# Kernel optimization log

Hardware: AMD Instinct MI355X
Metric: run time of the kernel (lower is better)

Reference implementation:

```python
import jax, jax.numpy as jnp
import numpy as np

B, S, D_IN, D_OUT, H = 4, 2048, 1024, 1024, 16
HD = D_OUT // H  # head_dim = 64


def setup_inputs() -> dict:
    key = jax.random.key(0)
    ks = jax.random.split(key, 7)
    sd_in = 1.0 / np.sqrt(D_IN)
    sd_out = 1.0 / np.sqrt(D_OUT)
    return {
        "x": jax.random.normal(ks[0], (B, S, D_IN), dtype=jnp.float32),
        # weights stored [in, out] so y = x @ W (equivalent to torch Linear)
        "wq": jax.random.uniform(ks[1], (D_IN, D_OUT), jnp.float32, -sd_in, sd_in),
        "wk": jax.random.uniform(ks[2], (D_IN, D_OUT), jnp.float32, -sd_in, sd_in),
        "wv": jax.random.uniform(ks[3], (D_IN, D_OUT), jnp.float32, -sd_in, sd_in),
        "wo": jax.random.uniform(ks[4], (D_OUT, D_OUT), jnp.float32, -sd_out, sd_out),
        "bo": jax.random.uniform(ks[5], (D_OUT,), jnp.float32, -sd_out, sd_out),
    }


def reference(x, wq, wk, wv, wo, bo):
    b, n, _ = x.shape
    # project and split heads: [b, h, n, hd]
    q = (x @ wq).reshape(b, n, H, HD).transpose(0, 2, 1, 3)
    k = (x @ wk).reshape(b, n, H, HD).transpose(0, 2, 1, 3)
    v = (x @ wv).reshape(b, n, H, HD).transpose(0, 2, 1, 3)
    scale = 1.0 / jnp.sqrt(jnp.asarray(HD, dtype=x.dtype))
    scores = jnp.einsum('bhqd,bhkd->bhqk', q, k) * scale  # [b,h,n,n]
    causal = jnp.tril(jnp.ones((n, n), dtype=bool))
    scores = jnp.where(causal, scores, -jnp.inf)
    attn = jax.nn.softmax(scores, axis=-1)
    # dropout p=0.0 -> identity
    ctx = jnp.einsum('bhqk,bhkd->bhqd', attn, v)
    ctx = ctx.transpose(0, 2, 1, 3).reshape(b, n, D_OUT)
    return ctx @ wo + bo
```

## Files before the change

### kernel.cpp

```cpp
#include <hip/hip_runtime.h>

#define DEVINL __device__ __forceinline__

typedef __attribute__((ext_vector_type(8))) short s8v;
typedef __attribute__((ext_vector_type(4))) float f4v;
typedef __attribute__((ext_vector_type(16))) float f16v;
typedef __attribute__((ext_vector_type(8))) __bf16 bf8v;
typedef __attribute__((ext_vector_type(4))) unsigned int u4v;

static constexpr int SEQ = 2048;
static constexpr int DIM = 1024;
static constexpr int NH = 16;

DEVINL unsigned short f2bf(float f) {
  unsigned int u = __builtin_bit_cast(unsigned int, f);
  u += 0x7FFFu + ((u >> 16) & 1u);
  return (unsigned short)(u >> 16);
}

DEVINL void gl_lds16(const void* g, void* l) {
  __builtin_amdgcn_global_load_lds((__attribute__((address_space(1))) void*)g,
                                   (__attribute__((address_space(3))) void*)l,
                                   16, 0, 0);
}

DEVINL f4v mfma16(s8v a, s8v b, f4v c) {
  return __builtin_amdgcn_mfma_f32_16x16x32_bf16(__builtin_bit_cast(bf8v, a),
                                                 __builtin_bit_cast(bf8v, b),
                                                 c, 0, 0, 0);
}

DEVINL f16v mfma32(s8v a, s8v b, f16v c) {
  return __builtin_amdgcn_mfma_f32_32x32x16_bf16(__builtin_bit_cast(bf8v, a),
                                                 __builtin_bit_cast(bf8v, b),
                                                 c, 0, 0, 0);
}

DEVINL unsigned cvtpk(float lo, float hi) {
  unsigned r;
  asm("v_cvt_pk_bf16_f32 %0, %1, %2" : "=v"(r) : "v"(lo), "v"(hi));
  return r;
}

DEVINL void plswap(unsigned& a, unsigned& b) {
#if __has_builtin(__builtin_amdgcn_permlane32_swap)
  typedef int i2v __attribute__((ext_vector_type(2)));
  i2v r = __builtin_amdgcn_permlane32_swap((int)a, (int)b, false, false);
  a = (unsigned)r[0]; b = (unsigned)r[1];
#else
  asm volatile("v_permlane32_swap_b32 %0, %1" : "+v"(a), "+v"(b));
#endif
}

DEVINL s8v mkfrag(unsigned w0, unsigned w1, unsigned w2, unsigned w3) {
  u4v t = {w0, w1, w2, w3};
  return __builtin_bit_cast(s8v, t);
}

__global__ __launch_bounds__(256) void k_cvt(const float* __restrict__ in,
                                             unsigned short* __restrict__ outp) {
  const int i = blockIdx.x * 256 + threadIdx.x;
  const f4v* p = (const f4v*)in + (size_t)i * 2;
  f4v a = p[0], b = p[1];
  s8v o;
  o[0] = (short)f2bf(a[0]); o[1] = (short)f2bf(a[1]);
  o[2] = (short)f2bf(a[2]); o[3] = (short)f2bf(a[3]);
  o[4] = (short)f2bf(b[0]); o[5] = (short)f2bf(b[1]);
  o[6] = (short)f2bf(b[2]); o[7] = (short)f2bf(b[3]);
  ((s8v*)outp)[i] = o;
}

__global__ __launch_bounds__(256) void k_twt(const float* __restrict__ w0, const float* __restrict__ w1,
                                             const float* __restrict__ w2, const float* __restrict__ w3,
                                             unsigned short* __restrict__ o0, unsigned short* __restrict__ o1,
                                             unsigned short* __restrict__ o2, unsigned short* __restrict__ o3) {
  __shared__ float tile[32][33];
  const float* w = blockIdx.z == 0 ? w0 : blockIdx.z == 1 ? w1 : blockIdx.z == 2 ? w2 : w3;
  unsigned short* o = blockIdx.z == 0 ? o0 : blockIdx.z == 1 ? o1 : blockIdx.z == 2 ? o2 : o3;
  const int r0 = blockIdx.y * 32, c0 = blockIdx.x * 32;
  const int tx = threadIdx.x & 31, ty = threadIdx.x >> 5;
#pragma unroll
  for (int i = 0; i < 32; i += 8) tile[ty + i][tx] = w[(r0 + ty + i) * DIM + c0 + tx];
  __syncthreads();
#pragma unroll
  for (int i = 0; i < 32; i += 8) o[(c0 + ty + i) * DIM + r0 + tx] = f2bf(tile[tx][ty + i]);
}

DEVINL void stage128(const unsigned short* __restrict__ A, const unsigned short* __restrict__ Bt,
                     int m0, int n0, int k0, char* Ab, char* Bb, int tid) {
#pragma unroll
  for (int ld = 0; ld < 4; ++ld) {
    const int c = ld * 256 + tid;
    const int row = c >> 3;
    const int csw = ((c & 7) ^ (row & 7)) * 8;
    gl_lds16(A + (size_t)(m0 + row) * 1024 + k0 + csw, Ab + c * 16);
    gl_lds16(Bt + (size_t)(n0 + row) * 1024 + k0 + csw, Bb + c * 16);
  }
}

DEVINL void gemm_compute_tile(char* Ar, char* Br, f4v acc[4][4],
                              int l15, int lg, int wm, int wn) {
#pragma unroll
  for (int kk = 0; kk < 2; ++kk) {
    s8v af[4], bfr[4];
    const int kb2 = (kk * 32 + lg * 8) * 2;
#pragma unroll
    for (int mf = 0; mf < 4; ++mf) {
      const int row = wm * 64 + mf * 16 + l15;
      af[mf] = *(const s8v*)(Ar + row * 128 + (kb2 ^ ((row & 7) << 4)));
    }
#pragma unroll
    for (int nf = 0; nf < 4; ++nf) {
      const int row = wn * 64 + nf * 16 + l15;
      bfr[nf] = *(const s8v*)(Br + row * 128 + (kb2 ^ ((row & 7) << 4)));
    }
#pragma unroll
    for (int mf = 0; mf < 4; ++mf)
#pragma unroll
      for (int nf = 0; nf < 4; ++nf) acc[mf][nf] = mfma16(af[mf], bfr[nf], acc[mf][nf]);
  }
}

DEVINL void gemm_ring(const unsigned short* __restrict__ A, const unsigned short* __restrict__ Bt,
                      int m0, int n0, char* smem, f4v acc[4][4]) {
  const int tid = threadIdx.x;
  const int lane = tid & 63, l15 = lane & 15, lg = lane >> 4;
  const int wm = (tid >> 6) >> 1, wn = (tid >> 6) & 1;
  constexpr int NT = 16;

  stage128(A, Bt, m0, n0, 0, smem, smem + 32768, tid);

  for (int t = 0; t < NT - 1; ++t) {
    const int nb = (t + 1) & 1;
    stage128(A, Bt, m0, n0, (t + 1) * 64, smem + nb * 16384, smem + 32768 + nb * 16384, tid);
    asm volatile("s_waitcnt vmcnt(8)" ::: "memory");
    __builtin_amdgcn_s_barrier();
    __builtin_amdgcn_sched_barrier(0);
    const int cb = t & 1;
    gemm_compute_tile(smem + cb * 16384, smem + 32768 + cb * 16384, acc, l15, lg, wm, wn);
    asm volatile("s_waitcnt lgkmcnt(0)" ::: "memory");
    __builtin_amdgcn_sched_barrier(0);
    __builtin_amdgcn_s_barrier();
  }
  asm volatile("s_waitcnt vmcnt(0)" ::: "memory");
  __builtin_amdgcn_s_barrier();
  __builtin_amdgcn_sched_barrier(0);
  gemm_compute_tile(smem + ((NT - 1) & 1) * 16384, smem + 32768 + ((NT - 1) & 1) * 16384,
                    acc, l15, lg, wm, wn);
}

__global__ __launch_bounds__(256) void k_qkv(const unsigned short* __restrict__ xb,
                                             const unsigned short* __restrict__ wqt,
                                             const unsigned short* __restrict__ wkt,
                                             const unsigned short* __restrict__ wvt,
                                             unsigned short* __restrict__ q,
                                             unsigned short* __restrict__ k,
                                             unsigned short* __restrict__ v) {
  __shared__ __align__(16) char smem[65536];
  const int wgid = (blockIdx.x & 7) * 192 + (blockIdx.x >> 3);
  const int m0 = (wgid / 24) * 128;
  const int rem = wgid % 24;
  const int which = rem >> 3;
  const int n0 = (rem & 7) * 128;
  const unsigned short* Bt = which == 0 ? wqt : which == 1 ? wkt : wvt;
  unsigned short* C = which == 0 ? q : which == 1 ? k : v;
  const float oscale = which == 0 ? 0.125f * 1.44269504f : 1.0f;
  f4v acc[4][4];
  const f4v z = {0.f, 0.f, 0.f, 0.f};
#pragma unroll
  for (int a = 0; a < 4; ++a)
#pragma unroll
    for (int b = 0; b < 4; ++b) acc[a][b] = z;
  gemm_ring(xb, Bt, m0, n0, smem, acc);
  const int lane = threadIdx.x & 63, l15 = lane & 15, lg = lane >> 4;
  const int wm = (threadIdx.x >> 6) >> 1, wn = (threadIdx.x >> 6) & 1;
#pragma unroll
  for (int mf = 0; mf < 4; ++mf)
#pragma unroll
    for (int nf = 0; nf < 4; ++nf)
#pragma unroll
      for (int r = 0; r < 4; ++r) {
        const int row = m0 + wm * 64 + mf * 16 + lg * 4 + r;
        const int col = n0 + wn * 64 + nf * 16 + l15;
        C[(size_t)row * 1024 + col] = f2bf(acc[mf][nf][r] * oscale);
      }
}

__global__ __launch_bounds__(256) void k_oproj(const unsigned short* __restrict__ ctx,
                                               const unsigned short* __restrict__ wot,
                                               const float* __restrict__ bo,
                                               float* __restrict__ outp) {
  __shared__ __align__(16) char smem[65536];
  const int wgid = (blockIdx.x & 7) * 64 + (blockIdx.x >> 3);
  const int m0 = (wgid >> 3) * 128;
  const int n0 = (wgid & 7) * 128;
  f4v acc[4][4];
  const f4v z = {0.f, 0.f, 0.f, 0.f};
#pragma unroll
  for (int a = 0; a < 4; ++a)
#pragma unroll
    for (int b = 0; b < 4; ++b) acc[a][b] = z;
  gemm_ring(ctx, wot, m0, n0, smem, acc);
  const int lane = threadIdx.x & 63, l15 = lane & 15, lg = lane >> 4;
  const int wm = (threadIdx.x >> 6) >> 1, wn = (threadIdx.x >> 6) & 1;
#pragma unroll
  for (int nf = 0; nf < 4; ++nf) {
    const int col = n0 + wn * 64 + nf * 16 + l15;
    const float bias = bo[col];
#pragma unroll
    for (int mf = 0; mf < 4; ++mf)
#pragma unroll
      for (int r = 0; r < 4; ++r) {
        const int row = m0 + wm * 64 + mf * 16 + lg * 4 + r;
        outp[(size_t)row * 1024 + col] = acc[mf][nf][r] + bias;
      }
  }
}

__global__ __launch_bounds__(256) void k_tv(const unsigned short* __restrict__ v,
                                            unsigned short* __restrict__ vt) {
  __shared__ unsigned short tile[64][65];
  const int b = blockIdx.z, h = blockIdx.y, s0 = blockIdx.x * 64;
  const int t = threadIdx.x;
#pragma unroll
  for (int i = 0; i < 16; ++i) {
    const int s = i * 4 + (t >> 6), d = t & 63;
    tile[s][d] = v[(size_t)(b * SEQ + s0 + s) * 1024 + h * 64 + d];
  }
  __syncthreads();
#pragma unroll
  for (int i = 0; i < 16; ++i) {
    const int d = i * 4 + (t >> 6), s = t & 63;
    vt[(size_t)((b * NH + h) * 64 + d) * SEQ + s0 + s] = tile[s][d];
  }
}

DEVINL void stage_kv(const unsigned short* __restrict__ kbase,
                     const unsigned short* __restrict__ vbase,
                     int kv0, char* Ks, char* Vs, int tid) {
#pragma unroll
  for (int i = 0; i < 2; ++i) {
    const int c = i * 256 + tid;
    const int row = c >> 3;
    const int csw = ((c & 7) ^ (row & 7)) * 8;
    gl_lds16(kbase + (size_t)(kv0 + row) * 1024 + csw, Ks + c * 16);
    gl_lds16(vbase + (size_t)row * SEQ + kv0 + csw, Vs + c * 16);
  }
}

__global__ __launch_bounds__(256) void k_attn(const unsigned short* __restrict__ q,
                                              const unsigned short* __restrict__ kg,
                                              const unsigned short* __restrict__ vt,
                                              unsigned short* __restrict__ ctx) {
  __shared__ __align__(16) char smem[32768];
  const int b = blockIdx.z, h = blockIdx.y, pair = blockIdx.x;
  const int tid = threadIdx.x, lane = tid & 63, w = tid >> 6;
  const int l31 = lane & 31, hi = lane >> 5;

  const unsigned short* kbase = kg + (size_t)b * SEQ * 1024 + h * 64;
  const unsigned short* vbase = vt + (size_t)((b * NH + h) * 64) * SEQ;

  f16v z16;
#pragma unroll
  for (int i = 0; i < 16; ++i) z16[i] = 0.f;

  for (int seg = 0; seg < 2; ++seg) {
    const int qi = seg == 0 ? pair : 15 - pair;
    const int qbb = qi * 128;
    const int qg = qbb + w * 32 + l31;
    const unsigned short* qp = q + (size_t)(b * SEQ + qg) * 1024 + h * 64;
    s8v qf[4];
#pragma unroll
    for (int kd = 0; kd < 4; ++kd) qf[kd] = *(const s8v*)(qp + kd * 16 + hi * 8);

    f16v o0 = z16, o1 = z16;
    float m = -3e38f, lsum = 0.f;
    const int nt = qi * 2 + 2;

    __syncthreads();
    stage_kv(kbase, vbase, 0, smem, smem + 16384, tid);

    for (int t = 0; t < nt; ++t) {
      const int kv0 = t * 64;
      char* Ks = smem + (t & 1) * 8192;
      char* Vs = smem + 16384 + (t & 1) * 8192;
      __syncthreads();
      if (t + 1 < nt)
        stage_kv(kbase, vbase, kv0 + 64, smem + ((t + 1) & 1) * 8192,
                 smem + 16384 + ((t + 1) & 1) * 8192, tid);
      if (kv0 > qbb + w * 32 + 31) continue;

      f16v s0 = z16, s1 = z16;
#pragma unroll
      for (int kd = 0; kd < 4; ++kd) {
        const int off = kd * 32 + hi * 16;
        const int r0 = l31, r1 = 32 + l31;
        const s8v kf0 = *(const s8v*)(Ks + r0 * 128 + (off ^ ((r0 & 7) << 4)));
        const s8v kf1 = *(const s8v*)(Ks + r1 * 128 + (off ^ ((r1 & 7) << 4)));
        s0 = mfma32(kf0, qf[kd], s0);
        s1 = mfma32(kf1, qf[kd], s1);
      }

      const bool needmask = (kv0 + 63 > qbb + w * 32);
      const int crel = qg - kv0;
      float tmax = -3e38f;
#pragma unroll
      for (int r = 0; r < 16; ++r) {
        const int kvloc = (r & 3) + 8 * (r >> 2) + 4 * hi;
        float v0 = s0[r], v1 = s1[r];
        if (needmask) {
          if (kvloc > crel) v0 = -3e38f;
          if (kvloc + 32 > crel) v1 = -3e38f;
        }
        s0[r] = v0; s1[r] = v1;
        tmax = fmaxf(tmax, fmaxf(v0, v1));
      }
      tmax = fmaxf(tmax, __shfl_xor(tmax, 32));

      const bool grew = tmax > m + 8.f;
      const float mnew = grew ? tmax : m;
      const float corr = __builtin_amdgcn_exp2f(m - mnew);
      m = mnew;

      float rs = 0.f;
#pragma unroll
      for (int r = 0; r < 16; ++r) {
        const float e0 = __builtin_amdgcn_exp2f(s0[r] - m);
        const float e1 = __builtin_amdgcn_exp2f(s1[r] - m);
        s0[r] = e0; s1[r] = e1;
        rs += e0 + e1;
      }
      rs += __shfl_xor(rs, 32);
      lsum = lsum * corr + rs;
      if (__any(grew)) { o0 *= corr; o1 *= corr; }

      unsigned a0 = cvtpk(s0[0], s0[1]), b0 = cvtpk(s0[4], s0[5]); plswap(a0, b0);
      unsigned a1 = cvtpk(s0[2], s0[3]), b1 = cvtpk(s0[6], s0[7]); plswap(a1, b1);
      const s8v f0 = mkfrag(a0, a1, b0, b1);
      unsigned a2 = cvtpk(s0[8], s0[9]), b2 = cvtpk(s0[12], s0[13]); plswap(a2, b2);
      unsigned a3 = cvtpk(s0[10], s0[11]), b3 = cvtpk(s0[14], s0[15]); plswap(a3, b3);
      const s8v f1 = mkfrag(a2, a3, b2, b3);
      unsigned a4 = cvtpk(s1[0], s1[1]), b4 = cvtpk(s1[4], s1[5]); plswap(a4, b4);
      unsigned a5 = cvtpk(s1[2], s1[3]), b5 = cvtpk(s1[6], s1[7]); plswap(a5, b5);
      const s8v f2 = mkfrag(a4, a5, b4, b5);
      unsigned a6 = cvtpk(s1[8], s1[9]), b6 = cvtpk(s1[12], s1[13]); plswap(a6, b6);
      unsigned a7 = cvtpk(s1[10], s1[11]), b7 = cvtpk(s1[14], s1[15]); plswap(a7, b7);
      const s8v f3 = mkfrag(a6, a7, b6, b7);

#pragma unroll
      for (int ks = 0; ks < 4; ++ks) {
        const s8v pb = ks == 0 ? f0 : ks == 1 ? f1 : ks == 2 ? f2 : f3;
        const int off = ks * 32 + hi * 16;
        const int rd0 = l31, rd1 = 32 + l31;
        const s8v v0 = *(const s8v*)(Vs + rd0 * 128 + (off ^ ((rd0 & 7) << 4)));
        const s8v v1 = *(const s8v*)(Vs + rd1 * 128 + (off ^ ((rd1 & 7) << 4)));
        o0 = mfma32(v0, pb, o0);
        o1 = mfma32(v1, pb, o1);
      }
    }

    const float rl = 1.f / lsum;
    unsigned short* crow_p = ctx + (size_t)(b * SEQ + qg) * 1024 + h * 64;
#pragma unroll
    for (int r = 0; r < 16; ++r) {
      const int d = (r & 3) + 8 * (r >> 2) + 4 * hi;
      crow_p[d] = f2bf(o0[r] * rl);
      crow_p[32 + d] = f2bf(o1[r] * rl);
    }
  }
}

extern "C" void kernel_launch(void* const* d_in, const int* in_sizes, int n_in,
                              void* d_out, int out_size, void* d_ws, size_t ws_size,
                              hipStream_t stream) {
  (void)in_sizes; (void)n_in; (void)out_size; (void)ws_size;
  const float* x = (const float*)d_in[0];
  const float* wq = (const float*)d_in[1];
  const float* wk = (const float*)d_in[2];
  const float* wv = (const float*)d_in[3];
  const float* wo = (const float*)d_in[4];
  const float* bo = (const float*)d_in[5];
  float* outp = (float*)d_out;
  char* ws = (char*)d_ws;
  const size_t MB = 1ull << 20;
  unsigned short* xb  = (unsigned short*)(ws + 0 * MB);
  unsigned short* wqt = (unsigned short*)(ws + 16 * MB);
  unsigned short* wkt = (unsigned short*)(ws + 18 * MB);
  unsigned short* wvt = (unsigned short*)(ws + 20 * MB);
  unsigned short* wot = (unsigned short*)(ws + 22 * MB);
  unsigned short* qb_ = (unsigned short*)(ws + 24 * MB);
  unsigned short* kb_ = (unsigned short*)(ws + 40 * MB);
  unsigned short* vb_ = (unsigned short*)(ws + 56 * MB);
  unsigned short* vtb = (unsigned short*)(ws + 72 * MB);
  unsigned short* ctx = (unsigned short*)(ws + 88 * MB);

  k_cvt<<<4096, 256, 0, stream>>>(x, xb);
  k_twt<<<dim3(32, 32, 4), 256, 0, stream>>>(wq, wk, wv, wo, wqt, wkt, wvt, wot);
  k_qkv<<<1536, 256, 0, stream>>>(xb, wqt, wkt, wvt, qb_, kb_, vb_);
  k_tv<<<dim3(32, 16, 4), 256, 0, stream>>>(vb_, vtb);
  k_attn<<<dim3(8, 16, 4), 256, 0, stream>>>(qb_, kb_, vtb, ctx);
  k_oproj<<<512, 256, 0, stream>>>(ctx, wot, bo, outp);
}
```

Baseline: 256.1 us.

## Use 128x256 tiles with 3-stage LDS ring and 8 waves for projection GEMMs

The QKV and output-projection GEMMs move from 128x128 tiles with 256 threads and double buffering to 128x256 tiles with 512 threads (8 waves, 2x4 layout). A triple-buffered 144KB dynamic LDS ring keeps two K-steps in flight, and s_setprio is raised around the MFMA bursts. The goal is more operand reuse per loaded A tile and better hiding of global-to-LDS latency. The cost is that the large LDS footprint allows only one workgroup per CU, and the grid has fewer, larger blocks, which could leave CUs unevenly loaded at the tail.

```diff
diff --git a/kernel.cpp b/kernel.cpp
--- a/kernel.cpp
+++ b/kernel.cpp
@@ -86,82 +86,94 @@
   for (int i = 0; i < 32; i += 8) o[(c0 + ty + i) * DIM + r0 + tx] = f2bf(tile[tx][ty + i]);
 }
 
-DEVINL void stage128(const unsigned short* __restrict__ A, const unsigned short* __restrict__ Bt,
-                     int m0, int n0, int k0, char* Ab, char* Bb, int tid) {
-#pragma unroll
-  for (int ld = 0; ld < 4; ++ld) {
-    const int c = ld * 256 + tid;
+static constexpr int SLOT = 49152;
+static constexpr int RING_LDS = 147456;
+
+DEVINL void stage_ab(const unsigned short* __restrict__ A, const unsigned short* __restrict__ Bt,
+                     int m0, int n0, int k0, char* slot, int tid) {
+#pragma unroll
+  for (int ld = 0; ld < 2; ++ld) {
+    const int c = ld * 512 + tid;
     const int row = c >> 3;
     const int csw = ((c & 7) ^ (row & 7)) * 8;
-    gl_lds16(A + (size_t)(m0 + row) * 1024 + k0 + csw, Ab + c * 16);
-    gl_lds16(Bt + (size_t)(n0 + row) * 1024 + k0 + csw, Bb + c * 16);
-  }
-}
-
-DEVINL void gemm_compute_tile(char* Ar, char* Br, f4v acc[4][4],
-                              int l15, int lg, int wm, int wn) {
-#pragma unroll
-  for (int kk = 0; kk < 2; ++kk) {
-    s8v af[4], bfr[4];
-    const int kb2 = (kk * 32 + lg * 8) * 2;
-#pragma unroll
-    for (int mf = 0; mf < 4; ++mf) {
-      const int row = wm * 64 + mf * 16 + l15;
-      af[mf] = *(const s8v*)(Ar + row * 128 + (kb2 ^ ((row & 7) << 4)));
-    }
-#pragma unroll
-    for (int nf = 0; nf < 4; ++nf) {
-      const int row = wn * 64 + nf * 16 + l15;
-      bfr[nf] = *(const s8v*)(Br + row * 128 + (kb2 ^ ((row & 7) << 4)));
-    }
-#pragma unroll
-    for (int mf = 0; mf < 4; ++mf)
-#pragma unroll
-      for (int nf = 0; nf < 4; ++nf) acc[mf][nf] = mfma16(af[mf], bfr[nf], acc[mf][nf]);
-  }
-}
-
-DEVINL void gemm_ring(const unsigned short* __restrict__ A, const unsigned short* __restrict__ Bt,
-                      int m0, int n0, char* smem, f4v acc[4][4]) {
+    gl_lds16(A + (size_t)(m0 + row) * 1024 + k0 + csw, slot + c * 16);
+  }
+#pragma unroll
+  for (int ld = 0; ld < 4; ++ld) {
+    const int c = ld * 512 + tid;
+    const int row = c >> 3;
+    const int csw = ((c & 7) ^ (row & 7)) * 8;
+    gl_lds16(Bt + (size_t)(n0 + row) * 1024 + k0 + csw, slot + 16384 + c * 16);
+  }
+}
+
+DEVINL void gemm_ring3(const unsigned short* __restrict__ A, const unsigned short* __restrict__ Bt,
+                       int m0, int n0, char* smem, f4v acc[4][4]) {
   const int tid = threadIdx.x;
   const int lane = tid & 63, l15 = lane & 15, lg = lane >> 4;
-  const int wm = (tid >> 6) >> 1, wn = (tid >> 6) & 1;
+  const int wid = tid >> 6, wm = wid >> 2, wn = wid & 3;
   constexpr int NT = 16;
 
-  stage128(A, Bt, m0, n0, 0, smem, smem + 32768, tid);
-
-  for (int t = 0; t < NT - 1; ++t) {
-    const int nb = (t + 1) & 1;
-    stage128(A, Bt, m0, n0, (t + 1) * 64, smem + nb * 16384, smem + 32768 + nb * 16384, tid);
-    asm volatile("s_waitcnt vmcnt(8)" ::: "memory");
+  stage_ab(A, Bt, m0, n0, 0, smem, tid);
+  stage_ab(A, Bt, m0, n0, 64, smem + SLOT, tid);
+
+  for (int t = 0; t < NT; ++t) {
+    if (t + 2 < NT) {
+      stage_ab(A, Bt, m0, n0, (t + 2) * 64, smem + ((t + 2) % 3) * SLOT, tid);
+      asm volatile("s_waitcnt vmcnt(12)" ::: "memory");
+    } else if (t + 2 == NT) {
+      asm volatile("s_waitcnt vmcnt(6)" ::: "memory");
+    } else {
+      asm volatile("s_waitcnt vmcnt(0)" ::: "memory");
+    }
     __builtin_amdgcn_s_barrier();
     __builtin_amdgcn_sched_barrier(0);
-    const int cb = t & 1;
-    gemm_compute_tile(smem + cb * 16384, smem + 32768 + cb * 16384, acc, l15, lg, wm, wn);
-    asm volatile("s_waitcnt lgkmcnt(0)" ::: "memory");
+
+    char* Ar = smem + (t % 3) * SLOT;
+    char* Br = Ar + 16384;
+#pragma unroll
+    for (int kk = 0; kk < 2; ++kk) {
+      s8v af[4];
+#pragma unroll
+      for (int mf = 0; mf < 4; ++mf) {
+        const int row = wm * 64 + mf * 16 + l15;
+        af[mf] = *(const s8v*)(Ar + row * 128 + ((kk * 64 + lg * 16) ^ ((row & 7) << 4)));
+      }
+#pragma unroll
+      for (int nh = 0; nh < 2; ++nh) {
+        s8v bfr[2];
+#pragma unroll
+        for (int j = 0; j < 2; ++j) {
+          const int row = wn * 64 + (nh * 2 + j) * 16 + l15;
+          bfr[j] = *(const s8v*)(Br + row * 128 + ((kk * 64 + lg * 16) ^ ((row & 7) << 4)));
+        }
+        __builtin_amdgcn_s_setprio(1);
+#pragma unroll
+        for (int mf = 0; mf < 4; ++mf) {
+          acc[mf][nh * 2 + 0] = mfma16(af[mf], bfr[0], acc[mf][nh * 2 + 0]);
+          acc[mf][nh * 2 + 1] = mfma16(af[mf], bfr[1], acc[mf][nh * 2 + 1]);
+        }
+        __builtin_amdgcn_s_setprio(0);
+      }
+    }
     __builtin_amdgcn_sched_barrier(0);
     __builtin_amdgcn_s_barrier();
   }
-  asm volatile("s_waitcnt vmcnt(0)" ::: "memory");
-  __builtin_amdgcn_s_barrier();
-  __builtin_amdgcn_sched_barrier(0);
-  gemm_compute_tile(smem + ((NT - 1) & 1) * 16384, smem + 32768 + ((NT - 1) & 1) * 16384,
-                    acc, l15, lg, wm, wn);
-}
-
-__global__ __launch_bounds__(256) void k_qkv(const unsigned short* __restrict__ xb,
-                                             const unsigned short* __restrict__ wqt,
-                                             const unsigned short* __restrict__ wkt,
-                                             const unsigned short* __restrict__ wvt,
-                                             unsigned short* __restrict__ q,
-                                             unsigned short* __restrict__ k,
-                                             unsigned short* __restrict__ v) {
-  __shared__ __align__(16) char smem[65536];
-  const int wgid = (blockIdx.x & 7) * 192 + (blockIdx.x >> 3);
-  const int m0 = (wgid / 24) * 128;
-  const int rem = wgid % 24;
-  const int which = rem >> 3;
-  const int n0 = (rem & 7) * 128;
+}
+
+__global__ __launch_bounds__(512, 2) void k_qkv(const unsigned short* __restrict__ xb,
+                                                const unsigned short* __restrict__ wqt,
+                                                const unsigned short* __restrict__ wkt,
+                                                const unsigned short* __restrict__ wvt,
+                                                unsigned short* __restrict__ q,
+                                                unsigned short* __restrict__ k,
+                                                unsigned short* __restrict__ v) {
+  extern __shared__ __align__(16) char smem[];
+  const int wgid = (blockIdx.x & 7) * 96 + (blockIdx.x >> 3);
+  const int m0 = (wgid / 12) * 128;
+  const int rem = wgid % 12;
+  const int which = rem >> 2;
+  const int n0 = (rem & 3) * 256;
   const unsigned short* Bt = which == 0 ? wqt : which == 1 ? wkt : wvt;
   unsigned short* C = which == 0 ? q : which == 1 ? k : v;
   const float oscale = which == 0 ? 0.125f * 1.44269504f : 1.0f;
@@ -171,9 +183,9 @@
   for (int a = 0; a < 4; ++a)
 #pragma unroll
     for (int b = 0; b < 4; ++b) acc[a][b] = z;
-  gemm_ring(xb, Bt, m0, n0, smem, acc);
+  gemm_ring3(xb, Bt, m0, n0, smem, acc);
   const int lane = threadIdx.x & 63, l15 = lane & 15, lg = lane >> 4;
-  const int wm = (threadIdx.x >> 6) >> 1, wn = (threadIdx.x >> 6) & 1;
+  const int wid = threadIdx.x >> 6, wm = wid >> 2, wn = wid & 3;
 #pragma unroll
   for (int mf = 0; mf < 4; ++mf)
 #pragma unroll
@@ -186,23 +198,23 @@
       }
 }
 
-__global__ __launch_bounds__(256) void k_oproj(const unsigned short* __restrict__ ctx,
-                                               const unsigned short* __restrict__ wot,
-                                               const float* __restrict__ bo,
-                                               float* __restrict__ outp) {
-  __shared__ __align__(16) char smem[65536];
-  const int wgid = (blockIdx.x & 7) * 64 + (blockIdx.x >> 3);
-  const int m0 = (wgid >> 3) * 128;
-  const int n0 = (wgid & 7) * 128;
+__global__ __launch_bounds__(512, 2) void k_oproj(const unsigned short* __restrict__ ctx,
+                                                  const unsigned short* __restrict__ wot,
+                                                  const float* __restrict__ bo,
+                                                  float* __restrict__ outp) {
+  extern __shared__ __align__(16) char smem[];
+  const int wgid = (blockIdx.x & 7) * 32 + (blockIdx.x >> 3);
+  const int m0 = (wgid >> 2) * 128;
+  const int n0 = (wgid & 3) * 256;
   f4v acc[4][4];
   const f4v z = {0.f, 0.f, 0.f, 0.f};
 #pragma unroll
   for (int a = 0; a < 4; ++a)
 #pragma unroll
     for (int b = 0; b < 4; ++b) acc[a][b] = z;
-  gemm_ring(ctx, wot, m0, n0, smem, acc);
+  gemm_ring3(ctx, wot, m0, n0, smem, acc);
   const int lane = threadIdx.x & 63, l15 = lane & 15, lg = lane >> 4;
-  const int wm = (threadIdx.x >> 6) >> 1, wn = (threadIdx.x >> 6) & 1;
+  const int wid = threadIdx.x >> 6, wm = wid >> 2, wn = wid & 3;
 #pragma unroll
   for (int nf = 0; nf < 4; ++nf) {
     const int col = n0 + wn * 64 + nf * 16 + l15;
@@ -394,10 +406,13 @@
   unsigned short* vtb = (unsigned short*)(ws + 72 * MB);
   unsigned short* ctx = (unsigned short*)(ws + 88 * MB);
 
+  (void)hipFuncSetAttribute((const void*)k_qkv, hipFuncAttributeMaxDynamicSharedMemorySize, RING_LDS);
+  (void)hipFuncSetAttribute((const void*)k_oproj, hipFuncAttributeMaxDynamicSharedMemorySize, RING_LDS);
+
   k_cvt<<<4096, 256, 0, stream>>>(x, xb);
   k_twt<<<dim3(32, 32, 4), 256, 0, stream>>>(wq, wk, wv, wo, wqt, wkt, wvt, wot);
-  k_qkv<<<1536, 256, 0, stream>>>(xb, wqt, wkt, wvt, qb_, kb_, vb_);
+  k_qkv<<<768, 512, RING_LDS, stream>>>(xb, wqt, wkt, wvt, qb_, kb_, vb_);
   k_tv<<<dim3(32, 16, 4), 256, 0, stream>>>(vb_, vtb);
   k_attn<<<dim3(8, 16, 4), 256, 0, stream>>>(qb_, kb_, vtb, ctx);
-  k_oproj<<<512, 256, 0, stream>>>(ctx, wot, bo, outp);
-}
+  k_oproj<<<256, 512, RING_LDS, stream>>>(ctx, wot, bo, outp);
+}
```

Result: no change. 258.9 us (+1.1%).
